# Performance work log

Hardware: AMD Instinct MI355X
Metric: run time of the kernel (lower is better)

Reference implementation:

```python
import jax, jax.numpy as jnp
import numpy as np

B, S = 8, 1024          # sequences, tokens per sequence (batched prefill)
DIM = 2048
N_HEADS, N_KV_HEADS = 16, 8
HEAD_DIM = DIM // N_HEADS   # 128
N_REP = N_HEADS // N_KV_HEADS
BLOCK_SIZE = 16
NUM_BLOCKS = B * S // BLOCK_SIZE  # 512
T = B * S
ROPE_THETA = 10000.0


def apply_rotary_paged(x, positions):
    # x: [T, H, head_dim], positions: [T] int -- Llama-style interleaved rotary
    hd = x.shape[-1]
    inv_freq = 1.0 / (ROPE_THETA ** (jnp.arange(0, hd, 2, dtype=jnp.float32) / hd))  # [hd/2]
    ang = positions.astype(jnp.float32)[:, None] * inv_freq[None, :]                  # [T, hd/2]
    cos = jnp.cos(ang)[:, None, :]  # [T, 1, hd/2]
    sin = jnp.sin(ang)[:, None, :]
    xr, xi = x[..., 0::2], x[..., 1::2]
    out_r = xr * cos - xi * sin
    out_i = xr * sin + xi * cos
    return jnp.stack([out_r, out_i], axis=-1).reshape(x.shape).astype(x.dtype)


def setup_inputs() -> dict:
    key = jax.random.key(0)
    ks = jax.random.split(key, 6)
    std = 0.02
    x = jax.random.normal(ks[0], (T, DIM), dtype=jnp.float32)
    wq = jax.random.normal(ks[1], (DIM, N_HEADS * HEAD_DIM), dtype=jnp.float32) * std
    wk = jax.random.normal(ks[2], (DIM, N_KV_HEADS * HEAD_DIM), dtype=jnp.float32) * std
    wv = jax.random.normal(ks[3], (DIM, N_KV_HEADS * HEAD_DIM), dtype=jnp.float32) * std
    wo = jax.random.normal(ks[4], (N_HEADS * HEAD_DIM, DIM), dtype=jnp.float32) * std
    k_cache = jnp.zeros((NUM_BLOCKS, 1, N_KV_HEADS, BLOCK_SIZE, HEAD_DIM), dtype=jnp.float32)
    v_cache = jnp.zeros((NUM_BLOCKS, 1, N_KV_HEADS, BLOCK_SIZE, HEAD_DIM), dtype=jnp.float32)
    positions = jnp.tile(jnp.arange(S, dtype=jnp.int32), B)          # [T]
    tokens_per_seq = jnp.full((B,), S, dtype=jnp.int32)
    context_lengths = jnp.full((B,), S, dtype=jnp.int32)
    block_tables = jnp.arange(NUM_BLOCKS, dtype=jnp.int32).reshape(B, S // BLOCK_SIZE)
    return {"x": x, "wq": wq, "wk": wk, "wv": wv, "wo": wo,
            "k_cache": k_cache, "v_cache": v_cache,
            "positions": positions, "tokens_per_seq": tokens_per_seq,
            "context_lengths": context_lengths, "block_tables": block_tables,
            "layer_idx": 0}


def reference(x, wq, wk, wv, wo, k_cache, v_cache,
              positions, tokens_per_seq, context_lengths, block_tables, layer_idx):
    # QKV projections (Linear, no bias)
    xq = (x @ wq).reshape(T, N_HEADS, HEAD_DIM)
    xk = (x @ wk).reshape(T, N_KV_HEADS, HEAD_DIM)
    xv = (x @ wv).reshape(T, N_KV_HEADS, HEAD_DIM)
    xq = apply_rotary_paged(xq, positions)
    xk = apply_rotary_paged(xk, positions)

    # --- scatter new K/V into paged caches via block tables ---
    seq_ids = jnp.arange(T, dtype=jnp.int32) // S                 # [T]
    blk = block_tables[seq_ids, positions // BLOCK_SIZE]           # [T]
    off = positions % BLOCK_SIZE                                   # [T]
    k_cache = k_cache.at[blk, layer_idx, :, off, :].set(xk)        # [T,kvh,hd]
    v_cache = v_cache.at[blk, layer_idx, :, off, :].set(xv)

    # --- gather full K/V per sequence from the paged caches ---
    kpos = jnp.arange(S, dtype=jnp.int32)                          # [S]
    blk_g = block_tables[:, kpos // BLOCK_SIZE]                    # [B, S]
    off_g = jnp.broadcast_to(kpos % BLOCK_SIZE, (B, S))            # [B, S]
    gk = k_cache[blk_g, layer_idx, :, off_g, :]                    # [B, S, kvh, hd]
    gv = v_cache[blk_g, layer_idx, :, off_g, :]

    # GQA: repeat_interleave kv heads to n_heads
    gk = jnp.repeat(gk, N_REP, axis=2)                             # [B, S, h, hd]
    gv = jnp.repeat(gv, N_REP, axis=2)

    q = xq.reshape(B, S, N_HEADS, HEAD_DIM)
    scale = 1.0 / np.sqrt(HEAD_DIM).astype(np.float32)
    scores = jnp.einsum('bqhd,bkhd->bhqk', q, gk) * scale          # [B,h,S,S]

    # causal mask using token positions (prefill)
    q_pos = positions.reshape(B, S)
    mask = q_pos[:, None, :, None] < kpos[None, None, None, :]     # [B,1,S,S]
    scores = jnp.where(mask, -jnp.inf, scores)

    probs = jax.nn.softmax(scores.astype(jnp.float32), axis=-1).astype(q.dtype)
    attn = jnp.einsum('bhqk,bkhd->bqhd', probs, gv)                # [B,S,h,hd]
    out = attn.reshape(T, N_HEADS * HEAD_DIM) @ wo                 # resid dropout = identity (eval)
    return out
```

## Files before the change

kernel.cpp:

```cpp
#include <hip/hip_runtime.h>
#include <stdint.h>

#define TTOK  8192
#define DIMM  2048
#define NH    16
#define NKV   8
#define HD    128
#define SEQ   1024
#define BATCH 8
#define BLKSZ 16

typedef unsigned short u16;
typedef __attribute__((ext_vector_type(8))) short bfrag;
typedef __attribute__((ext_vector_type(4))) float f32x4;

__device__ __forceinline__ float bf2f(u16 u) {
  unsigned int v = ((unsigned int)u) << 16;
  float f; __builtin_memcpy(&f, &v, 4); return f;
}
__device__ __forceinline__ u16 f2bf(float f) {
  unsigned int v; __builtin_memcpy(&v, &f, 4);
  v = v + 0x7FFFu + ((v >> 16) & 1u);
  return (u16)(v >> 16);
}

__device__ __forceinline__ void gll16(const void* g, void* l) {
  __builtin_amdgcn_global_load_lds(
      (__attribute__((address_space(1))) void*)(g),
      (__attribute__((address_space(3))) void*)(l), 16, 0, 0);
}

__device__ __forceinline__ void lds_barrier() {
  asm volatile("s_waitcnt lgkmcnt(0)" ::: "memory");
  __builtin_amdgcn_sched_barrier(0);
  __builtin_amdgcn_s_barrier();
}

__global__ __launch_bounds__(256) void f32_to_bf16(const float* __restrict__ in,
                                                   u16* __restrict__ out, size_t n) {
  size_t i = ((size_t)blockIdx.x * 256 + threadIdx.x) * 8;
  if (i >= n) return;
  float4 a = *(const float4*)(in + i);
  float4 b = *(const float4*)(in + i + 4);
  union { u16 o[8]; uint4 v; } u;
  u.o[0] = f2bf(a.x); u.o[1] = f2bf(a.y); u.o[2] = f2bf(a.z); u.o[3] = f2bf(a.w);
  u.o[4] = f2bf(b.x); u.o[5] = f2bf(b.y); u.o[6] = f2bf(b.z); u.o[7] = f2bf(b.w);
  *(uint4*)(out + i) = u.v;
}

__global__ __launch_bounds__(256) void ktranspose_f(const float* __restrict__ in,
                                                    u16* __restrict__ out, int K, int N) {
  __shared__ __align__(16) u16 tile[64 * 65];
  int n0 = blockIdx.x * 64, k0 = blockIdx.y * 64;
  int tx = threadIdx.x & 63, ty = threadIdx.x >> 6;
  for (int r = 0; r < 16; ++r) {
    int kk = r * 4 + ty;
    tile[kk * 65 + tx] = f2bf(in[(size_t)(k0 + kk) * N + n0 + tx]);
  }
  __syncthreads();
  for (int r = 0; r < 16; ++r) {
    int nn = r * 4 + ty;
    out[(size_t)(n0 + nn) * K + k0 + tx] = tile[tx * 65 + nn];
  }
}

template <typename OutT>
__global__ __launch_bounds__(512, 2) void gemm_bt8(const u16* __restrict__ A,
                                                   const u16* __restrict__ Bt,
                                                   OutT* __restrict__ C,
                                                   int M, int N, int K) {
  __shared__ __align__(16) u16 AS[2][256 * 64];
  __shared__ __align__(16) u16 BS[2][256 * 64];
  (void)M;
  int tid = threadIdx.x;
  int w = tid >> 6, lane = tid & 63, quad = lane >> 4, l15 = lane & 15;
  int wr = w >> 2, wc = w & 3;

  int nwg = gridDim.x * gridDim.y;
  int id = blockIdx.y * gridDim.x + blockIdx.x;
  int swz = (id & 7) * (nwg >> 3) + (id >> 3);
  int bx = swz % gridDim.x, by = swz / gridDim.x;
  int m0 = by * 256, n0 = bx * 256;

  size_t Kb = (size_t)K * 2;
  int nt = K >> 6;

  int s_lr = lane >> 3;
  int s_lo = ((lane & 7) ^ s_lr) * 16;
  auto stageA = [&](int half, int tk, char* As) {
    int rloc = half * 128 + w * 16;
    const char* src = (const char*)A + (size_t)(m0 + rloc + s_lr) * Kb + (size_t)tk * 128 + s_lo;
    char* dst = As + rloc * 128 + lane * 16;
    gll16(src, dst);
    gll16(src + 8 * Kb, dst + 1024);
  };
  auto stageB = [&](int half, int tk, char* Bs) {
    int rloc = half * 128 + w * 16;
    const char* src = (const char*)Bt + (size_t)(n0 + rloc + s_lr) * Kb + (size_t)tk * 128 + s_lo;
    char* dst = Bs + rloc * 128 + lane * 16;
    gll16(src, dst);
    gll16(src + 8 * Kb, dst + 1024);
  };

  f32x4 acc[2][4][2][2];
#pragma unroll
  for (int mh = 0; mh < 2; ++mh)
#pragma unroll
    for (int f = 0; f < 4; ++f)
#pragma unroll
      for (int nh = 0; nh < 2; ++nh)
#pragma unroll
        for (int g = 0; g < 2; ++g) acc[mh][f][nh][g] = (f32x4){0.f, 0.f, 0.f, 0.f};

  stageA(0, 0, (char*)AS[0]); stageA(1, 0, (char*)AS[0]);
  stageB(0, 0, (char*)BS[0]); stageB(1, 0, (char*)BS[0]);
  if (nt > 1) {
    stageA(0, 1, (char*)AS[1]); stageA(1, 1, (char*)AS[1]);
    stageB(0, 1, (char*)BS[1]); stageB(1, 1, (char*)BS[1]);
    asm volatile("s_waitcnt vmcnt(8)" ::: "memory");
  } else {
    asm volatile("s_waitcnt vmcnt(0)" ::: "memory");
  }
  lds_barrier();

  int rswz = (l15 & 7) << 4;
  int aRow = wr * 64 + l15;
  int bRow = wc * 32 + l15;

  for (int t = 0; t < nt; ++t) {
    char* As = (char*)AS[t & 1];
    char* Bs = (char*)BS[t & 1];
    bool pre = (t + 2 < nt);
    bfrag aA[4][2], aB0[2][2], aB1[2][2];

#pragma unroll
    for (int f = 0; f < 4; ++f)
#pragma unroll
      for (int kk = 0; kk < 2; ++kk)
        aA[f][kk] = *(const bfrag*)(As + (aRow + f * 16) * 128 + ((kk * 64 + quad * 16) ^ rswz));
#pragma unroll
    for (int g = 0; g < 2; ++g)
#pragma unroll
      for (int kk = 0; kk < 2; ++kk)
        aB0[g][kk] = *(const bfrag*)(Bs + (bRow + g * 16) * 128 + ((kk * 64 + quad * 16) ^ rswz));
    __builtin_amdgcn_s_setprio(1);
#pragma unroll
    for (int f = 0; f < 4; ++f)
#pragma unroll
      for (int g = 0; g < 2; ++g)
#pragma unroll
        for (int kk = 0; kk < 2; ++kk)
          acc[0][f][0][g] = __builtin_amdgcn_mfma_f32_16x16x32_bf16(aA[f][kk], aB0[g][kk], acc[0][f][0][g], 0, 0, 0);
    __builtin_amdgcn_s_setprio(0);
    lds_barrier();

    if (pre) { stageA(0, t + 2, As); stageB(0, t + 2, Bs); }
#pragma unroll
    for (int g = 0; g < 2; ++g)
#pragma unroll
      for (int kk = 0; kk < 2; ++kk)
        aB1[g][kk] = *(const bfrag*)(Bs + (bRow + 128 + g * 16) * 128 + ((kk * 64 + quad * 16) ^ rswz));
    __builtin_amdgcn_s_setprio(1);
#pragma unroll
    for (int f = 0; f < 4; ++f)
#pragma unroll
      for (int g = 0; g < 2; ++g)
#pragma unroll
        for (int kk = 0; kk < 2; ++kk)
          acc[0][f][1][g] = __builtin_amdgcn_mfma_f32_16x16x32_bf16(aA[f][kk], aB1[g][kk], acc[0][f][1][g], 0, 0, 0);
    __builtin_amdgcn_s_setprio(0);
    lds_barrier();

    if (pre) stageB(1, t + 2, Bs);
#pragma unroll
    for (int f = 0; f < 4; ++f)
#pragma unroll
      for (int kk = 0; kk < 2; ++kk)
        aA[f][kk] = *(const bfrag*)(As + (aRow + 128 + f * 16) * 128 + ((kk * 64 + quad * 16) ^ rswz));
    __builtin_amdgcn_s_setprio(1);
#pragma unroll
    for (int f = 0; f < 4; ++f)
#pragma unroll
      for (int g = 0; g < 2; ++g)
#pragma unroll
        for (int kk = 0; kk < 2; ++kk)
          acc[1][f][1][g] = __builtin_amdgcn_mfma_f32_16x16x32_bf16(aA[f][kk], aB1[g][kk], acc[1][f][1][g], 0, 0, 0);
    __builtin_amdgcn_s_setprio(0);
    lds_barrier();

    if (pre) stageA(1, t + 2, As);
    __builtin_amdgcn_s_setprio(1);
#pragma unroll
    for (int f = 0; f < 4; ++f)
#pragma unroll
      for (int g = 0; g < 2; ++g)
#pragma unroll
        for (int kk = 0; kk < 2; ++kk)
          acc[1][f][0][g] = __builtin_amdgcn_mfma_f32_16x16x32_bf16(aA[f][kk], aB0[g][kk], acc[1][f][0][g], 0, 0, 0);
    __builtin_amdgcn_s_setprio(0);
    if (pre)
      asm volatile("s_waitcnt vmcnt(8)" ::: "memory");
    else if (t + 1 < nt)
      asm volatile("s_waitcnt vmcnt(0)" ::: "memory");
    lds_barrier();
  }

#pragma unroll
  for (int mh = 0; mh < 2; ++mh)
#pragma unroll
    for (int f = 0; f < 4; ++f)
#pragma unroll
      for (int nh = 0; nh < 2; ++nh)
#pragma unroll
        for (int g = 0; g < 2; ++g)
#pragma unroll
          for (int rr = 0; rr < 4; ++rr) {
            int row = m0 + wr * 64 + mh * 128 + f * 16 + quad * 4 + rr;
            int col = n0 + wc * 32 + nh * 128 + g * 16 + l15;
            float v = acc[mh][f][nh][g][rr];
            if constexpr (__is_same(OutT, float))
              C[(size_t)row * N + col] = v;
            else
              C[(size_t)row * N + col] = f2bf(v);
          }
}

__global__ __launch_bounds__(256) void rope_scatter(const u16* __restrict__ xqkv,
                                                    const int* __restrict__ positions,
                                                    const int* __restrict__ btab,
                                                    u16* __restrict__ qb,
                                                    u16* __restrict__ kb,
                                                    u16* __restrict__ vbuf) {
  int t = blockIdx.x;
  int tid = threadIdx.x;
  int b = t >> 10, srow = t & 1023;
  int pos = positions[t];
  int blk = btab[b * (SEQ / BLKSZ) + (pos >> 4)];
  int off = pos & (BLKSZ - 1);
  int c0 = tid * 16;

  struct __align__(16) { uint4 a, bq; } vv, oo;
  const u16* src = xqkv + (size_t)t * 4096 + c0;
  vv.a  = *(const uint4*)src;
  vv.bq = *(const uint4*)(src + 8);
  const u16* v = (const u16*)&vv;
  u16* o = (u16*)&oo;

  if (c0 < 3072) {
    int dbase = c0 & 127;
    float fpos = (float)pos;
    for (int j = 0; j < 8; ++j) {
      int i = (dbase >> 1) + j;
      float inv = exp2f(-(float)i * (13.287712379549449f / 64.0f));
      float ang = fpos * inv;
      float sn, cs;
      sincosf(ang, &sn, &cs);
      float fr = bf2f(v[2 * j]), fi = bf2f(v[2 * j + 1]);
      o[2 * j]     = f2bf(fr * cs - fi * sn);
      o[2 * j + 1] = f2bf(fr * sn + fi * cs);
    }
  } else {
    for (int j = 0; j < 16; ++j) o[j] = v[j];
  }

  u16* dst;
  if (c0 < 2048) {
    int head = c0 >> 7, d0 = c0 & 127;
    dst = qb + (((size_t)(b * NH + head)) * SEQ + srow) * HD + d0;
  } else if (c0 < 3072) {
    int cc = c0 - 2048;
    int kvh = cc >> 7, d0 = cc & 127;
    dst = kb + (((size_t)(blk * NKV + kvh) * BLKSZ + off)) * HD + d0;
  } else {
    int cc = c0 - 3072;
    int kvh = cc >> 7, d0 = cc & 127;
    dst = vbuf + (((size_t)(blk * NKV + kvh) * BLKSZ + off)) * HD + d0;
  }
  *(uint4*)dst = oo.a;
  *(uint4*)(dst + 8) = oo.bq;
}

#define KVT 64
#define KS_STRIDE 272
#define VT_STRIDE 144
#define PS_STRIDE 144

__global__ __launch_bounds__(512) void attn_kernel(const u16* __restrict__ Q,
                                                   const u16* __restrict__ Kc,
                                                   const u16* __restrict__ Vc,
                                                   const int* __restrict__ positions,
                                                   const int* __restrict__ btab,
                                                   u16* __restrict__ O) {
  __shared__ __align__(16) u16 Ks[KVT * (KS_STRIDE / 2)];
  __shared__ __align__(16) u16 Vt[HD * (VT_STRIDE / 2)];
  __shared__ __align__(16) u16 Ps[8 * 16 * (PS_STRIDE / 2)];
  const float SM_SCALE = 0.08838834764831845f;
  const float LOG2E    = 1.4426950408889634f;
  const float C1       = SM_SCALE * LOG2E;
  const float NEGBIG   = -30000.0f;
  const float NEGINIT  = -1e30f;
  const float DEFER2   = 8.0f * LOG2E;

  int tid = threadIdx.x;
  int wave = tid >> 6, lane = tid & 63, quad = lane >> 4, l15 = lane & 15;
  int bid = blockIdx.x;
  int bh = bid >> 2, pr = bid & 3;
  int b = bh >> 4, h = bh & 15, kvh = h >> 1;
  const int* btrow = btab + b * (SEQ / BLKSZ);

  char* KsB = (char*)Ks;
  char* VtB = (char*)Vt;
  char* myPsB = (char*)Ps + wave * 16 * PS_STRIDE;

  int tokA = tid >> 4;
  int tokB = tokA + 32;
  int dgK  = tid & 15;
  int tokV = (tid & 31) * 2;
  int vd0  = (tid >> 5) * 8;

  uint4 kr0, kr1, vr0, vr1;

  auto load_tile = [&](int kti) {
    int i0 = kti >> 4;
    int b0 = btrow[i0], b1 = btrow[i0 + 1], b2 = btrow[i0 + 2], b3 = btrow[i0 + 3];
    const u16* KA = Kc + ((size_t)(((tokA < 16) ? b0 : b1) * NKV + kvh) * BLKSZ + (tokA & 15)) * HD + dgK * 8;
    const u16* KB = Kc + ((size_t)(((tokB < 48) ? b2 : b3) * NKV + kvh) * BLKSZ + (tokB & 15)) * HD + dgK * 8;
    kr0 = *(const uint4*)KA;
    kr1 = *(const uint4*)KB;
    int bv = (tokV < 16) ? b0 : (tokV < 32) ? b1 : (tokV < 48) ? b2 : b3;
    const u16* VA = Vc + ((size_t)(bv * NKV + kvh) * BLKSZ + (tokV & 15)) * HD + vd0;
    vr0 = *(const uint4*)VA;
    vr1 = *(const uint4*)(VA + HD);
  };

  for (int pass = 0; pass < 2; ++pass) {
    int yt = pass ? (7 - pr) : pr;
    int q0 = yt * 128;
    int qw = q0 + wave * 16;

    const u16* Qbase = Q + ((size_t)bh * SEQ + qw) * HD;

    bfrag aq[4];
#pragma unroll
    for (int kb2 = 0; kb2 < 4; ++kb2)
      aq[kb2] = *(const bfrag*)(Qbase + (size_t)l15 * HD + kb2 * 32 + quad * 8);

    int qpos[4];
#pragma unroll
    for (int r = 0; r < 4; ++r)
      qpos[r] = positions[(size_t)b * SEQ + qw + quad * 4 + r];

    f32x4 oa[8];
#pragma unroll
    for (int jd = 0; jd < 8; ++jd) oa[jd] = (f32x4){0.f, 0.f, 0.f, 0.f};
    float m2_i[4], l_i[4];
#pragma unroll
    for (int r = 0; r < 4; ++r) { m2_i[r] = NEGINIT; l_i[r] = 0.f; }

    int kend = q0 + 128;
    load_tile(0);

    for (int kt = 0; kt < kend; kt += KVT) {
      __syncthreads();
      *(uint4*)(KsB + tokA * KS_STRIDE + dgK * 16) = kr0;
      *(uint4*)(KsB + tokB * KS_STRIDE + dgK * 16) = kr1;
      {
        const u16* p0 = (const u16*)&vr0;
        const u16* p1 = (const u16*)&vr1;
#pragma unroll
        for (int jj = 0; jj < 8; ++jj) {
          unsigned int val = (unsigned int)p0[jj] | ((unsigned int)p1[jj] << 16);
          *(unsigned int*)(VtB + (vd0 + jj) * VT_STRIDE + tokV * 2) = val;
        }
      }
      __syncthreads();

      if (kt + KVT < kend) load_tile(kt + KVT);

      if (kt <= qw + 15) {
        f32x4 sa[4];
#pragma unroll
        for (int jn = 0; jn < 4; ++jn) sa[jn] = (f32x4){0.f, 0.f, 0.f, 0.f};
#pragma unroll
        for (int kb2 = 0; kb2 < 4; ++kb2) {
#pragma unroll
          for (int jn = 0; jn < 4; ++jn) {
            bfrag bk = *(const bfrag*)(KsB + (jn * 16 + l15) * KS_STRIDE + (kb2 * 4 + quad) * 16);
            sa[jn] = __builtin_amdgcn_mfma_f32_16x16x32_bf16(aq[kb2], bk, sa[jn], 0, 0, 0);
          }
        }

        float m2x[4];
#pragma unroll
        for (int r = 0; r < 4; ++r) {
#pragma unroll
          for (int jn = 0; jn < 4; ++jn) {
            float s = sa[jn][r];
            if (kt + jn * 16 + l15 > qpos[r]) s = NEGBIG;
            sa[jn][r] = s;
          }
          float m0 = fmaxf(fmaxf(sa[0][r], sa[1][r]), fmaxf(sa[2][r], sa[3][r]));
          m0 = fmaxf(m0, __shfl_xor(m0, 1, 64));
          m0 = fmaxf(m0, __shfl_xor(m0, 2, 64));
          m0 = fmaxf(m0, __shfl_xor(m0, 4, 64));
          m0 = fmaxf(m0, __shfl_xor(m0, 8, 64));
          m2x[r] = m0 * C1;
        }

        bool ok = (m2x[0] <= m2_i[0] + DEFER2) && (m2x[1] <= m2_i[1] + DEFER2) &&
                  (m2x[2] <= m2_i[2] + DEFER2) && (m2x[3] <= m2_i[3] + DEFER2);
        if (__all(ok)) {
#pragma unroll
          for (int r = 0; r < 4; ++r) {
            float rs = 0.f;
#pragma unroll
            for (int jn = 0; jn < 4; ++jn) {
              float pv = exp2f(sa[jn][r] * C1 - m2_i[r]);
              sa[jn][r] = pv;
              rs += pv;
            }
            rs += __shfl_xor(rs, 1, 64);
            rs += __shfl_xor(rs, 2, 64);
            rs += __shfl_xor(rs, 4, 64);
            rs += __shfl_xor(rs, 8, 64);
            l_i[r] += rs;
          }
        } else {
          float alpha[4];
#pragma unroll
          for (int r = 0; r < 4; ++r) {
            float m2n = fmaxf(m2_i[r], m2x[r]);
            float al = exp2f(m2_i[r] - m2n);
            float rs = 0.f;
#pragma unroll
            for (int jn = 0; jn < 4; ++jn) {
              float pv = exp2f(sa[jn][r] * C1 - m2n);
              sa[jn][r] = pv;
              rs += pv;
            }
            rs += __shfl_xor(rs, 1, 64);
            rs += __shfl_xor(rs, 2, 64);
            rs += __shfl_xor(rs, 4, 64);
            rs += __shfl_xor(rs, 8, 64);
            l_i[r] = l_i[r] * al + rs;
            m2_i[r] = m2n;
            alpha[r] = al;
          }
#pragma unroll
          for (int jd = 0; jd < 8; ++jd) {
            oa[jd][0] *= alpha[0];
            oa[jd][1] *= alpha[1];
            oa[jd][2] *= alpha[2];
            oa[jd][3] *= alpha[3];
          }
        }

#pragma unroll
        for (int r = 0; r < 4; ++r) {
          int q = quad * 4 + r;
#pragma unroll
          for (int jn = 0; jn < 4; ++jn)
            *(u16*)(myPsB + q * PS_STRIDE + (jn * 16 + l15) * 2) = f2bf(sa[jn][r]);
        }
        bfrag ap0 = *(const bfrag*)(myPsB + l15 * PS_STRIDE + quad * 16);
        bfrag ap1 = *(const bfrag*)(myPsB + l15 * PS_STRIDE + 64 + quad * 16);
#pragma unroll
        for (int jd = 0; jd < 8; ++jd) {
          int d = jd * 16 + l15;
          bfrag bv0 = *(const bfrag*)(VtB + d * VT_STRIDE + quad * 16);
          bfrag bv1 = *(const bfrag*)(VtB + d * VT_STRIDE + 64 + quad * 16);
          oa[jd] = __builtin_amdgcn_mfma_f32_16x16x32_bf16(ap0, bv0, oa[jd], 0, 0, 0);
          oa[jd] = __builtin_amdgcn_mfma_f32_16x16x32_bf16(ap1, bv1, oa[jd], 0, 0, 0);
        }
      }
    }

#pragma unroll
    for (int r = 0; r < 4; ++r) {
      float inv = 1.0f / fmaxf(l_i[r], 1e-30f);
      size_t trow = (size_t)b * SEQ + qw + quad * 4 + r;
#pragma unroll
      for (int jd = 0; jd < 8; ++jd)
        O[trow * 2048 + (size_t)h * HD + jd * 16 + l15] = f2bf(oa[jd][r] * inv);
    }
  }
}

extern "C" void kernel_launch(void* const* d_in, const int* in_sizes, int n_in,
                              void* d_out, int out_size, void* d_ws, size_t ws_size,
                              hipStream_t stream) {
  (void)in_sizes; (void)n_in; (void)out_size;
  const float* xf  = (const float*)d_in[0];
  const float* wqf = (const float*)d_in[1];
  const float* wkf = (const float*)d_in[2];
  const float* wvf = (const float*)d_in[3];
  const float* wof = (const float*)d_in[4];
  const int* positions = (const int*)d_in[7];
  const int* btab      = (const int*)d_in[10];
  float* out = (float*)d_out;

  u16* ws    = (u16*)d_ws;
  u16* woT   = ws;
  u16* wqkvT = woT + (size_t)2048 * 2048;
  u16* xbf   = wqkvT + (size_t)4096 * 2048;
  u16* xqkv  = xbf + (size_t)8192 * 2048;
  u16* qb    = xqkv + (size_t)8192 * 4096;
  u16* kbuf  = qb + (size_t)8192 * 2048;
  u16* vbuf  = kbuf + (size_t)8192 * 1024;
  u16* wsend = vbuf + (size_t)8192 * 1024;

  size_t base_elems = (size_t)(wsend - ws);
  size_t obuf_elems = (size_t)8192 * 2048;
  u16* obuf;
  if (ws_size >= (base_elems + obuf_elems) * sizeof(u16))
    obuf = wsend;
  else
    obuf = wqkvT;

  if (ws_size < base_elems * sizeof(u16)) return;

  f32_to_bf16<<<dim3(8192), 256, 0, stream>>>(xf, xbf, (size_t)8192 * 2048);
  ktranspose_f<<<dim3(32, 32), 256, 0, stream>>>(wqf, wqkvT, 2048, 2048);
  ktranspose_f<<<dim3(16, 32), 256, 0, stream>>>(wkf, wqkvT + (size_t)2048 * 2048, 2048, 1024);
  ktranspose_f<<<dim3(16, 32), 256, 0, stream>>>(wvf, wqkvT + (size_t)3072 * 2048, 2048, 1024);
  ktranspose_f<<<dim3(32, 32), 256, 0, stream>>>(wof, woT, 2048, 2048);
  gemm_bt8<u16><<<dim3(16, 32), 512, 0, stream>>>(xbf, wqkvT, xqkv, 8192, 4096, 2048);
  rope_scatter<<<dim3(8192), 256, 0, stream>>>(xqkv, positions, btab, qb, kbuf, vbuf);
  attn_kernel<<<dim3(512), 512, 0, stream>>>(qb, kbuf, vbuf, positions, btab, obuf);
  gemm_bt8<float><<<dim3(8, 32), 512, 0, stream>>>(obuf, woT, out, 8192, 2048, 2048);
}
```

Baseline: 560.9 us.

## Restructure GEMM to four-stage K=32 pipeline with one barrier per step

```diff
diff --git a/kernel.cpp b/kernel.cpp
--- a/kernel.cpp
+++ b/kernel.cpp
@@ -28,12 +28,6 @@
   __builtin_amdgcn_global_load_lds(
       (__attribute__((address_space(1))) void*)(g),
       (__attribute__((address_space(3))) void*)(l), 16, 0, 0);
-}
-
-__device__ __forceinline__ void lds_barrier() {
-  asm volatile("s_waitcnt lgkmcnt(0)" ::: "memory");
-  __builtin_amdgcn_sched_barrier(0);
-  __builtin_amdgcn_s_barrier();
 }
 
 __global__ __launch_bounds__(256) void f32_to_bf16(const float* __restrict__ in,
@@ -65,12 +59,12 @@
 }
 
 template <typename OutT>
-__global__ __launch_bounds__(512, 2) void gemm_bt8(const u16* __restrict__ A,
+__global__ __launch_bounds__(512, 2) void gemm_bt4(const u16* __restrict__ A,
                                                    const u16* __restrict__ Bt,
                                                    OutT* __restrict__ C,
                                                    int M, int N, int K) {
-  __shared__ __align__(16) u16 AS[2][256 * 64];
-  __shared__ __align__(16) u16 BS[2][256 * 64];
+  __shared__ __align__(16) u16 AS[4][256 * 32];
+  __shared__ __align__(16) u16 BS[4][256 * 32];
   (void)M;
   int tid = threadIdx.x;
   int w = tid >> 6, lane = tid & 63, quad = lane >> 4, l15 = lane & 15;
@@ -83,24 +77,21 @@
   int m0 = by * 256, n0 = bx * 256;
 
   size_t Kb = (size_t)K * 2;
-  int nt = K >> 6;
-
-  int s_lr = lane >> 3;
-  int s_lo = ((lane & 7) ^ s_lr) * 16;
-  auto stageA = [&](int half, int tk, char* As) {
-    int rloc = half * 128 + w * 16;
-    const char* src = (const char*)A + (size_t)(m0 + rloc + s_lr) * Kb + (size_t)tk * 128 + s_lo;
-    char* dst = As + rloc * 128 + lane * 16;
-    gll16(src, dst);
-    gll16(src + 8 * Kb, dst + 1024);
+  int nt = K >> 5;
+
+  int srow = w * 32 + (lane >> 2);
+  int gslot = ((lane & 3) ^ ((lane >> 2) & 3)) * 16;
+  auto stage = [&](int tk) {
+    int bsel = tk & 3;
+    char* Ad = (char*)AS[bsel] + (w * 2) * 1024 + lane * 16;
+    char* Bd = (char*)BS[bsel] + (w * 2) * 1024 + lane * 16;
+    const char* As0 = (const char*)A + (size_t)(m0 + srow) * Kb + (size_t)tk * 64 + gslot;
+    const char* Bs0 = (const char*)Bt + (size_t)(n0 + srow) * Kb + (size_t)tk * 64 + gslot;
+    gll16(As0, Ad);
+    gll16(As0 + 16 * Kb, Ad + 1024);
+    gll16(Bs0, Bd);
+    gll16(Bs0 + 16 * Kb, Bd + 1024);
   };
-  auto stageB = [&](int half, int tk, char* Bs) {
-    int rloc = half * 128 + w * 16;
-    const char* src = (const char*)Bt + (size_t)(n0 + rloc + s_lr) * Kb + (size_t)tk * 128 + s_lo;
-    char* dst = Bs + rloc * 128 + lane * 16;
-    gll16(src, dst);
-    gll16(src + 8 * Kb, dst + 1024);
-  };
 
   f32x4 acc[2][4][2][2];
 #pragma unroll
@@ -112,97 +103,52 @@
 #pragma unroll
         for (int g = 0; g < 2; ++g) acc[mh][f][nh][g] = (f32x4){0.f, 0.f, 0.f, 0.f};
 
-  stageA(0, 0, (char*)AS[0]); stageA(1, 0, (char*)AS[0]);
-  stageB(0, 0, (char*)BS[0]); stageB(1, 0, (char*)BS[0]);
-  if (nt > 1) {
-    stageA(0, 1, (char*)AS[1]); stageA(1, 1, (char*)AS[1]);
-    stageB(0, 1, (char*)BS[1]); stageB(1, 1, (char*)BS[1]);
-    asm volatile("s_waitcnt vmcnt(8)" ::: "memory");
-  } else {
-    asm volatile("s_waitcnt vmcnt(0)" ::: "memory");
-  }
-  lds_barrier();
-
-  int rswz = (l15 & 7) << 4;
-  int aRow = wr * 64 + l15;
-  int bRow = wc * 32 + l15;
+  stage(0); stage(1); stage(2);
+  asm volatile("s_waitcnt vmcnt(8)" ::: "memory");
+  __builtin_amdgcn_s_barrier();
+
+  int rdoff = ((quad ^ (l15 & 3)) << 4);
+  int aRowB = (wr * 64 + l15) * 64 + rdoff;
+  int bRowB = (wc * 32 + l15) * 64 + rdoff;
 
   for (int t = 0; t < nt; ++t) {
-    char* As = (char*)AS[t & 1];
-    char* Bs = (char*)BS[t & 1];
-    bool pre = (t + 2 < nt);
-    bfrag aA[4][2], aB0[2][2], aB1[2][2];
-
-#pragma unroll
-    for (int f = 0; f < 4; ++f)
-#pragma unroll
-      for (int kk = 0; kk < 2; ++kk)
-        aA[f][kk] = *(const bfrag*)(As + (aRow + f * 16) * 128 + ((kk * 64 + quad * 16) ^ rswz));
-#pragma unroll
-    for (int g = 0; g < 2; ++g)
-#pragma unroll
-      for (int kk = 0; kk < 2; ++kk)
-        aB0[g][kk] = *(const bfrag*)(Bs + (bRow + g * 16) * 128 + ((kk * 64 + quad * 16) ^ rswz));
+    const char* Ab = (const char*)AS[t & 3];
+    const char* Bb = (const char*)BS[t & 3];
+
+    bfrag aA[2][4], bB[2][2];
+#pragma unroll
+    for (int mh = 0; mh < 2; ++mh)
+#pragma unroll
+      for (int f = 0; f < 4; ++f)
+        aA[mh][f] = *(const bfrag*)(Ab + aRowB + (mh * 128 + f * 16) * 64);
+#pragma unroll
+    for (int nh = 0; nh < 2; ++nh)
+#pragma unroll
+      for (int g = 0; g < 2; ++g)
+        bB[nh][g] = *(const bfrag*)(Bb + bRowB + (nh * 128 + g * 16) * 64);
+
+    if (t + 3 < nt) stage(t + 3);
+
     __builtin_amdgcn_s_setprio(1);
 #pragma unroll
-    for (int f = 0; f < 4; ++f)
-#pragma unroll
-      for (int g = 0; g < 2; ++g)
-#pragma unroll
-        for (int kk = 0; kk < 2; ++kk)
-          acc[0][f][0][g] = __builtin_amdgcn_mfma_f32_16x16x32_bf16(aA[f][kk], aB0[g][kk], acc[0][f][0][g], 0, 0, 0);
+    for (int mh = 0; mh < 2; ++mh)
+#pragma unroll
+      for (int f = 0; f < 4; ++f)
+#pragma unroll
+        for (int nh = 0; nh < 2; ++nh)
+#pragma unroll
+          for (int g = 0; g < 2; ++g)
+            acc[mh][f][nh][g] = __builtin_amdgcn_mfma_f32_16x16x32_bf16(
+                aA[mh][f], bB[nh][g], acc[mh][f][nh][g], 0, 0, 0);
     __builtin_amdgcn_s_setprio(0);
-    lds_barrier();
-
-    if (pre) { stageA(0, t + 2, As); stageB(0, t + 2, Bs); }
-#pragma unroll
-    for (int g = 0; g < 2; ++g)
-#pragma unroll
-      for (int kk = 0; kk < 2; ++kk)
-        aB1[g][kk] = *(const bfrag*)(Bs + (bRow + 128 + g * 16) * 128 + ((kk * 64 + quad * 16) ^ rswz));
-    __builtin_amdgcn_s_setprio(1);
-#pragma unroll
-    for (int f = 0; f < 4; ++f)
-#pragma unroll
-      for (int g = 0; g < 2; ++g)
-#pragma unroll
-        for (int kk = 0; kk < 2; ++kk)
-          acc[0][f][1][g] = __builtin_amdgcn_mfma_f32_16x16x32_bf16(aA[f][kk], aB1[g][kk], acc[0][f][1][g], 0, 0, 0);
-    __builtin_amdgcn_s_setprio(0);
-    lds_barrier();
-
-    if (pre) stageB(1, t + 2, Bs);
-#pragma unroll
-    for (int f = 0; f < 4; ++f)
-#pragma unroll
-      for (int kk = 0; kk < 2; ++kk)
-        aA[f][kk] = *(const bfrag*)(As + (aRow + 128 + f * 16) * 128 + ((kk * 64 + quad * 16) ^ rswz));
-    __builtin_amdgcn_s_setprio(1);
-#pragma unroll
-    for (int f = 0; f < 4; ++f)
-#pragma unroll
-      for (int g = 0; g < 2; ++g)
-#pragma unroll
-        for (int kk = 0; kk < 2; ++kk)
-          acc[1][f][1][g] = __builtin_amdgcn_mfma_f32_16x16x32_bf16(aA[f][kk], aB1[g][kk], acc[1][f][1][g], 0, 0, 0);
-    __builtin_amdgcn_s_setprio(0);
-    lds_barrier();
-
-    if (pre) stageA(1, t + 2, As);
-    __builtin_amdgcn_s_setprio(1);
-#pragma unroll
-    for (int f = 0; f < 4; ++f)
-#pragma unroll
-      for (int g = 0; g < 2; ++g)
-#pragma unroll
-        for (int kk = 0; kk < 2; ++kk)
-          acc[1][f][0][g] = __builtin_amdgcn_mfma_f32_16x16x32_bf16(aA[f][kk], aB0[g][kk], acc[1][f][0][g], 0, 0, 0);
-    __builtin_amdgcn_s_setprio(0);
-    if (pre)
+
+    asm volatile("s_waitcnt lgkmcnt(0)" ::: "memory");
+    __builtin_amdgcn_sched_barrier(0);
+    if (t + 3 < nt)
       asm volatile("s_waitcnt vmcnt(8)" ::: "memory");
     else if (t + 1 < nt)
       asm volatile("s_waitcnt vmcnt(0)" ::: "memory");
-    lds_barrier();
+    __builtin_amdgcn_s_barrier();
   }
 
 #pragma unroll
@@ -524,8 +470,8 @@
   ktranspose_f<<<dim3(16, 32), 256, 0, stream>>>(wkf, wqkvT + (size_t)2048 * 2048, 2048, 1024);
   ktranspose_f<<<dim3(16, 32), 256, 0, stream>>>(wvf, wqkvT + (size_t)3072 * 2048, 2048, 1024);
   ktranspose_f<<<dim3(32, 32), 256, 0, stream>>>(wof, woT, 2048, 2048);
-  gemm_bt8<u16><<<dim3(16, 32), 512, 0, stream>>>(xbf, wqkvT, xqkv, 8192, 4096, 2048);
+  gemm_bt4<u16><<<dim3(16, 32), 512, 0, stream>>>(xbf, wqkvT, xqkv, 8192, 4096, 2048);
   rope_scatter<<<dim3(8192), 256, 0, stream>>>(xqkv, positions, btab, qb, kbuf, vbuf);
   attn_kernel<<<dim3(512), 512, 0, stream>>>(qb, kbuf, vbuf, positions, btab, obuf);
-  gemm_bt8<float><<<dim3(8, 32), 512, 0, stream>>>(obuf, woT, out, 8192, 2048, 2048);
-}
+  gemm_bt4<float><<<dim3(8, 32), 512, 0, stream>>>(obuf, woT, out, 8192, 2048, 2048);
+}
```

After: 533.7 us. 1.05x faster.
